# Kernel optimization log

Hardware: AMD Instinct MI355X
Metric: run time of the kernel (lower is better)

The kernel has to match this reference:

```python
import jax, jax.numpy as jnp
import numpy as np

CANDIDATE_SIZE = 1000
IOU_THRESHOLD = 0.5
SCORE_THRESHOLD = 0.3
N_PRIORS = 400000
N_CLASSES = 81


def setup_inputs() -> dict:
    key = jax.random.key(0)
    k1, k2, k3 = jax.random.split(key, 3)
    scores = jax.random.uniform(k1, (1, N_PRIORS, N_CLASSES), dtype=jnp.float32)
    # build valid xyxy boxes in roughly [0, 1.1]
    centers = jax.random.uniform(k2, (1, N_PRIORS, 2), dtype=jnp.float32)
    sizes = jax.random.uniform(k3, (1, N_PRIORS, 2), dtype=jnp.float32) * 0.2 + 0.01
    boxes = jnp.concatenate([centers - sizes / 2, centers + sizes / 2], axis=-1)
    return {"scores": scores, "boxes": boxes}


def _iou_matrix(b):
    # b: [K, 4] xyxy -> [K, K] pairwise IoU
    x1 = jnp.maximum(b[:, None, 0], b[None, :, 0])
    y1 = jnp.maximum(b[:, None, 1], b[None, :, 1])
    x2 = jnp.minimum(b[:, None, 2], b[None, :, 2])
    y2 = jnp.minimum(b[:, None, 3], b[None, :, 3])
    inter = jnp.clip(x2 - x1, 0.0) * jnp.clip(y2 - y1, 0.0)
    area = (b[:, 2] - b[:, 0]) * (b[:, 3] - b[:, 1])
    union = area[:, None] + area[None, :] - inter
    return inter / jnp.maximum(union, 1e-9)


def reference(scores, boxes):
    s = scores[0]  # [N, C]
    b = boxes[0]   # [N, 4]
    cls_scores = s[:, 1:]                    # drop background class
    best = jnp.max(cls_scores, axis=1)       # [N] best foreground score
    labels = jnp.argmax(cls_scores, axis=1)  # [N] 0-based foreground label
    top_scores, top_idx = jax.lax.top_k(best, CANDIDATE_SIZE)  # sorted desc
    top_boxes = b[top_idx]                   # [K, 4]
    top_labels = labels[top_idx]             # [K]
    valid = top_scores > SCORE_THRESHOLD     # score-threshold mask (kept as mask, not filter, for static shapes)

    # batched_nms: offset boxes per class so cross-class IoU is 0
    offset = (top_labels.astype(top_boxes.dtype) * 4.0)[:, None]  # boxes span < 4
    iou = _iou_matrix(top_boxes + offset)    # [K, K]

    idx = jnp.arange(CANDIDATE_SIZE)

    def body(i, keep):
        # greedy suppression: candidates are already score-sorted
        suppress = keep[i] & (iou[i] > IOU_THRESHOLD) & (idx > i)
        return keep & ~suppress

    keep = jax.lax.fori_loop(0, CANDIDATE_SIZE, body, valid)  # [K] bool

    keepf = keep.astype(top_boxes.dtype)
    sel_boxes = top_boxes * keepf[:, None]          # zeroed where suppressed
    sel_probs = top_scores * keepf
    sel_labels = jnp.where(keep, top_labels + 1, 0)  # +1 to restore class ids
    return sel_boxes, sel_labels, sel_probs, keep
```

## Files before the change

### kernel.cpp

```cpp
#include <hip/hip_runtime.h>
#include <stdint.h>

#pragma clang fp contract(off)

#define N_PRIORS   400000
#define NCLS       81
#define TILE       128
#define RED_BLOCKS (N_PRIORS / TILE)
#define HGRID      512
#define CAND_CAP   8192
#define TOPK       1000
#define CM_CAP     448

#define OFF_CTRL    0
#define OFF_HIST0   64
#define OFF_HIST1   1088
#define OFF_HIST2   2112
#define OFF_RNZ     3200
#define OFF_VALID   3328
#define OFF_SLOT    4096
#define OFF_CSCORE  8192
#define OFF_CLABEL  12288
#define OFF_CRAW    16384
#define OFF_OBOX    32768
#define OFF_OAREA   49152
#define OFF_CAND    65536
#define OFF_CM      131072
#define OFF_KEYS    262144
#define OFF_LABELS  (OFF_KEYS + N_PRIORS * 8)

__device__ __forceinline__ uint32_t atomLoadU32(const uint32_t* p) {
  return __hip_atomic_load(p, __ATOMIC_RELAXED, __HIP_MEMORY_SCOPE_AGENT);
}
__device__ __forceinline__ uint64_t atomLoadU64(const uint64_t* p) {
  return __hip_atomic_load(p, __ATOMIC_RELAXED, __HIP_MEMORY_SCOPE_AGENT);
}
__device__ __forceinline__ void atomStoreU64(uint64_t* p, uint64_t v) {
  __hip_atomic_store(p, v, __ATOMIC_RELAXED, __HIP_MEMORY_SCOPE_AGENT);
}
__device__ __forceinline__ void atomStoreU32(uint32_t* p, uint32_t v) {
  __hip_atomic_store(p, v, __ATOMIC_RELAXED, __HIP_MEMORY_SCOPE_AGENT);
}

__device__ __forceinline__ void gload_lds16(const void* g, void* l) {
  __builtin_amdgcn_global_load_lds(
      (const __attribute__((address_space(1))) void*)g,
      (__attribute__((address_space(3))) void*)l, 16, 0, 0);
}

__device__ __forceinline__ void select_digit_wave(const uint32_t* hist, uint32_t k,
                                                  uint32_t prefix, int sh_dig,
                                                  uint32_t* ctrl, int lane) {
  uint32_t h[4];
  #pragma unroll
  for (int t = 0; t < 4; ++t) h[t] = atomLoadU32(&hist[255 - (4 * lane + t)]);
  uint32_t part = h[0] + h[1] + h[2] + h[3];
  uint32_t incl = part;
  #pragma unroll
  for (int d = 1; d < 64; d <<= 1) {
    uint32_t up = __shfl_up(incl, d);
    if (lane >= d) incl += up;
  }
  uint32_t excl = incl - part;
  if (excl < k && k <= incl) {
    uint32_t cum = excl;
    #pragma unroll
    for (int t = 0; t < 4; ++t) {
      if (cum + h[t] >= k) {
        ctrl[0] = prefix | ((uint32_t)(255 - (4 * lane + t)) << sh_dig);
        ctrl[1] = k - cum;
        break;
      }
      cum += h[t];
    }
  }
}

__global__ __launch_bounds__(256) void k_reduce(const float* __restrict__ scores,
                                                uint8_t* __restrict__ ws) {
  __shared__ __align__(16) float s_tile[TILE * NCLS];
  __shared__ uint32_t s_hist[256];
  __shared__ int s_last;
  uint32_t* ctrl  = (uint32_t*)(ws + OFF_CTRL);
  uint32_t* hist0 = (uint32_t*)(ws + OFF_HIST0);
  uint64_t* keys  = (uint64_t*)(ws + OFF_KEYS);
  int32_t*  labs  = (int32_t*)(ws + OFF_LABELS);
  const int tid = threadIdx.x;
  s_hist[tid] = 0;

  const float* src = scores + (size_t)blockIdx.x * (TILE * NCLS);
  {
    const int wave = tid >> 6, lane = tid & 63;
    const char* gbase = (const char*)src + lane * 16;
    char* lbase = (char*)s_tile;
    #pragma unroll
    for (int c = wave; c < 40; c += 4)
      gload_lds16(gbase + c * 1024, lbase + c * 1024);
  }
  if (tid < 32) {
    float4 v = ((const float4*)src)[2560 + tid];
    ((float4*)s_tile)[2560 + tid] = v;
  }
  __syncthreads();

  const int pl = tid >> 1, half = tid & 1;
  const float* row = s_tile + pl * NCLS + 1 + half * 40;
  float best = -1.0f; int lab = 0;
  #pragma unroll
  for (int c = 0; c < 40; ++c) {
    float v = row[c];
    if (v > best) { best = v; lab = c; }
  }
  lab += half * 40;
  float obst = __shfl_xor(best, 1);
  int   olab = __shfl_xor(lab, 1);
  float b0 = half ? obst : best;  int l0 = half ? olab : lab;
  float b1 = half ? best : obst;  int l1 = half ? lab  : olab;
  float fb = (b1 > b0) ? b1 : b0;
  int   fl = (b1 > b0) ? l1 : l0;

  if (half == 0) {
    int p = blockIdx.x * TILE + pl;
    uint32_t bits = __float_as_uint(fb);
    keys[p] = ((uint64_t)bits << 32) | (uint32_t)(~(uint32_t)p);
    labs[p] = fl;
    atomicAdd(&s_hist[bits >> 24], 1u);
  }
  __syncthreads();
  uint32_t h = s_hist[tid];
  if (h) atomicAdd(&hist0[tid], h);
  __syncthreads();
  if (tid == 0) {
    int r = blockIdx.x & 7;
    uint32_t target = (RED_BLOCKS >> 3) + ((uint32_t)r < (RED_BLOCKS & 7) ? 1u : 0u);
    int last = 0;
    if (atomicAdd(&ctrl[8 + r], 1u) == target - 1u)
      last = (atomicAdd(&ctrl[3], 1u) == 7u);
    s_last = last;
  }
  __syncthreads();
  if (s_last && tid < 64)
    select_digit_wave(hist0, TOPK, 0u, 24, ctrl, tid);
}

template <int P>
__global__ __launch_bounds__(256) void k_hist(uint8_t* __restrict__ ws) {
  __shared__ uint32_t s_hist[256];
  __shared__ int s_last;
  uint32_t* ctrl = (uint32_t*)(ws + OFF_CTRL);
  uint32_t* hist = (uint32_t*)(ws + (P == 1 ? OFF_HIST1 : OFF_HIST2));
  const uint64_t* keys = (const uint64_t*)(ws + OFF_KEYS);
  const int tid = threadIdx.x;
  s_hist[tid] = 0;
  __syncthreads();
  const uint32_t prefix = ctrl[0];
  constexpr int SH_MATCH = 32 - 8 * P;
  constexpr int SH_DIG   = 24 - 8 * P;
  const uint32_t pm = prefix >> SH_MATCH;
  for (int i = blockIdx.x * 256 + tid; i < N_PRIORS; i += 256 * HGRID) {
    uint32_t bits = (uint32_t)(keys[i] >> 32);
    if ((bits >> SH_MATCH) == pm) atomicAdd(&s_hist[(bits >> SH_DIG) & 255u], 1u);
  }
  __syncthreads();
  uint32_t h = s_hist[tid];
  if (h) atomicAdd(&hist[tid], h);
  __syncthreads();
  if (tid == 0) s_last = (atomicAdd(&ctrl[3 + P], 1u) == (uint32_t)(HGRID - 1));
  __syncthreads();
  if (s_last && tid < 64)
    select_digit_wave(hist, ctrl[1], prefix, SH_DIG, ctrl, tid);
}

__global__ __launch_bounds__(256) void k_compact(uint8_t* __restrict__ ws) {
  uint32_t* ctrl = (uint32_t*)(ws + OFF_CTRL);
  const uint64_t* keys = (const uint64_t*)(ws + OFF_KEYS);
  uint64_t* cand = (uint64_t*)(ws + OFF_CAND);
  const uint32_t thr = ctrl[0];
  const int tid = threadIdx.x;
  for (int i = blockIdx.x * 256 + tid; i < N_PRIORS; i += 256 * HGRID) {
    uint64_t kk = keys[i];
    if ((uint32_t)(kk >> 32) >= thr) {
      uint32_t pos = atomicAdd(&ctrl[2], 1u);
      if (pos < CAND_CAP) cand[pos] = kk;
    }
  }
}

__global__ __launch_bounds__(256) void k_rank(const float* __restrict__ boxes,
                                              uint8_t* __restrict__ ws) {
  uint32_t* ctrl = (uint32_t*)(ws + OFF_CTRL);
  const uint64_t* cand = (const uint64_t*)(ws + OFF_CAND);
  const int32_t* labs = (const int32_t*)(ws + OFF_LABELS);
  float*   cscore = (float*)(ws + OFF_CSCORE);
  int32_t* clabel = (int32_t*)(ws + OFF_CLABEL);
  float*   craw   = (float*)(ws + OFF_CRAW);
  float*   obox   = (float*)(ws + OFF_OBOX);
  float*   oarea  = (float*)(ws + OFF_OAREA);
  uint64_t* validm = (uint64_t*)(ws + OFF_VALID);
  uint32_t c2 = ctrl[2];
  const uint32_t n = (c2 < CAND_CAP) ? c2 : CAND_CAP;
  const uint32_t j = blockIdx.x;
  if (j >= n) return;
  const uint64_t kj = cand[j];
  const int tid = threadIdx.x;
  uint32_t cnt = 0;
  for (uint32_t i = tid; i < n; i += 256) cnt += (cand[i] > kj) ? 1u : 0u;
  __shared__ uint32_t red[256];
  red[tid] = cnt;
  __syncthreads();
  #pragma unroll
  for (int s = 128; s > 0; s >>= 1) {
    if (tid < s) red[tid] += red[tid + s];
    __syncthreads();
  }
  if (tid == 0) {
    uint32_t rank = red[0];
    if (rank < TOPK) {
      uint32_t idx = ~(uint32_t)kj;
      float sc = __uint_as_float((uint32_t)(kj >> 32));
      int lab = labs[idx];
      float bx0 = boxes[idx * 4 + 0];
      float bx1 = boxes[idx * 4 + 1];
      float bx2 = boxes[idx * 4 + 2];
      float bx3 = boxes[idx * 4 + 3];
      float off = (float)lab * 4.0f;
      float o0 = bx0 + off, o1 = bx1 + off, o2 = bx2 + off, o3 = bx3 + off;
      cscore[rank] = sc;
      clabel[rank] = lab;
      craw[rank * 4 + 0] = bx0; craw[rank * 4 + 1] = bx1;
      craw[rank * 4 + 2] = bx2; craw[rank * 4 + 3] = bx3;
      obox[rank * 4 + 0] = o0;  obox[rank * 4 + 1] = o1;
      obox[rank * 4 + 2] = o2;  obox[rank * 4 + 3] = o3;
      oarea[rank] = (o2 - o0) * (o3 - o1);
      if (sc > 0.3f)
        atomicOr((unsigned long long*)&validm[rank >> 6], 1ull << (rank & 63));
    }
  }
}

__global__ __launch_bounds__(256) void k_iou_nms(float* __restrict__ out,
                                                 uint8_t* __restrict__ ws) {
  __shared__ uint64_t s_words[16];
  __shared__ uint32_t s_slotsh;
  __shared__ int s_last;
  __shared__ uint64_t s_keep[16];
  __shared__ uint16_t s_slot[TOPK];
  __shared__ uint64_t s_cm[CM_CAP * 16];

  uint32_t* ctrl = (uint32_t*)(ws + OFF_CTRL);
  const float* obox  = (const float*)(ws + OFF_OBOX);
  const float* oarea = (const float*)(ws + OFF_OAREA);
  uint64_t* CM  = (uint64_t*)(ws + OFF_CM);
  uint64_t* rnz = (uint64_t*)(ws + OFF_RNZ);
  uint32_t* slotmap = (uint32_t*)(ws + OFF_SLOT);
  const uint64_t* validm = (const uint64_t*)(ws + OFF_VALID);
  const float*   cscore = (const float*)(ws + OFF_CSCORE);
  const int32_t* clabel = (const int32_t*)(ws + OFF_CLABEL);
  const float*   craw   = (const float*)(ws + OFF_CRAW);

  const int i = blockIdx.x;
  const int tid = threadIdx.x;
  const float bi0 = obox[i * 4 + 0], bi1 = obox[i * 4 + 1];
  const float bi2 = obox[i * 4 + 2], bi3 = obox[i * 4 + 3];
  const float ai = oarea[i];
  #pragma unroll
  for (int k = 0; k < 4; ++k) {
    int j = tid + 256 * k;
    const float4 bj = ((const float4*)obox)[j];
    float x1 = fmaxf(bi0, bj.x);
    float y1 = fmaxf(bi1, bj.y);
    float x2 = fminf(bi2, bj.z);
    float y2 = fminf(bi3, bj.w);
    float iw = fmaxf(x2 - x1, 0.0f);
    float ih = fmaxf(y2 - y1, 0.0f);
    float inter = iw * ih;
    float uni = ai + oarea[j] - inter;
    float iou = inter / fmaxf(uni, 1e-9f);
    bool pred = (iou > 0.5f) && (j > i) && (j < TOPK);
    uint64_t m = __ballot(pred);
    if ((tid & 63) == 0) s_words[(tid >> 6) + 4 * k] = m;
  }
  __syncthreads();
  if (tid == 0) {
    uint64_t any = 0;
    #pragma unroll
    for (int w = 0; w < 16; ++w) any |= s_words[w];
    uint32_t sl = 0xFFFFFFFFu;
    if (any) {
      sl = atomicAdd(&ctrl[7], 1u);
      atomicOr((unsigned long long*)&rnz[i >> 6], 1ull << (i & 63));
      atomStoreU32(&slotmap[i], sl + 1u);
    }
    s_slotsh = sl;
  }
  __syncthreads();
  {
    uint32_t sl = s_slotsh;
    if (sl != 0xFFFFFFFFu && tid < 16)
      atomStoreU64(&CM[(size_t)sl * 16 + tid], s_words[tid]);
  }
  __syncthreads();
  if (tid == 0) s_last = (atomicAdd(&ctrl[6], 1u) == (uint32_t)(TOPK - 1));
  __syncthreads();
  if (!s_last) return;

  uint32_t cmcnt = atomLoadU32(&ctrl[7]);
  uint32_t ncm = cmcnt < CM_CAP ? cmcnt : CM_CAP;
  for (int r = tid; r < TOPK; r += 256)
    s_slot[r] = (uint16_t)atomLoadU32(&slotmap[r]);
  for (uint32_t x = tid; x < ncm * 16; x += 256)
    s_cm[x] = atomLoadU64(&CM[x]);
  __syncthreads();

  if (tid < 64) {
    const int lane = tid;
    uint64_t keep = 0, rz = 0;
    if (lane < 16) {
      keep = validm[lane];
      rz = atomLoadU64(&rnz[lane]);
    }
    for (int w = 0; w < 16; ++w) {
      uint64_t rw = __shfl(rz, w);
      int start = 0;
      while (true) {
        uint64_t kw = __shfl(keep, w);
        uint64_t act = kw & rw;
        if (start) act &= (~0ull) << start;
        if (!act) break;
        int il = __builtin_ctzll(act);
        int row = w * 64 + il;
        uint32_t sv = s_slot[row];
        uint64_t m = 0;
        if (lane < 16 && sv) {
          uint32_t s = sv - 1u;
          m = (s < ncm) ? s_cm[s * 16 + lane]
                        : atomLoadU64(&CM[(size_t)s * 16 + lane]);
        }
        keep &= ~m;
        if (il >= 63) break;
        start = il + 1;
      }
    }
    if (lane < 16) s_keep[lane] = keep;
  }
  __syncthreads();

  for (int e = tid; e < 4000; e += 256) {
    int j = e >> 2;
    bool kp = (s_keep[j >> 6] >> (j & 63)) & 1ull;
    out[e] = kp ? craw[e] : 0.0f;
  }
  for (int j = tid; j < TOPK; j += 256) {
    bool kp = (s_keep[j >> 6] >> (j & 63)) & 1ull;
    out[4000 + j] = kp ? (float)(clabel[j] + 1) : 0.0f;
    out[5000 + j] = kp ? cscore[j] : 0.0f;
    out[6000 + j] = kp ? 1.0f : 0.0f;
  }
}

extern "C" void kernel_launch(void* const* d_in, const int* in_sizes, int n_in,
                              void* d_out, int out_size, void* d_ws, size_t ws_size,
                              hipStream_t stream) {
  const float* scores = (const float*)d_in[0];
  const float* boxes  = (const float*)d_in[1];
  float* out = (float*)d_out;
  uint8_t* ws = (uint8_t*)d_ws;

  (void)in_sizes; (void)n_in; (void)out_size; (void)ws_size;

  hipMemsetAsync(d_ws, 0, 65536, stream);
  k_reduce<<<RED_BLOCKS, 256, 0, stream>>>(scores, ws);
  k_hist<1><<<HGRID, 256, 0, stream>>>(ws);
  k_hist<2><<<HGRID, 256, 0, stream>>>(ws);
  k_compact<<<HGRID, 256, 0, stream>>>(ws);
  k_rank<<<CAND_CAP, 256, 0, stream>>>(boxes, ws);
  k_iou_nms<<<TOPK, 256, 0, stream>>>(out, ws);
}
```

Measured before the change: 265.6 us.

## Fuse post-reduce stages into one cooperative kernel with grid barriers

```diff
diff --git a/kernel.cpp b/kernel.cpp
--- a/kernel.cpp
+++ b/kernel.cpp
@@ -11,11 +11,12 @@
 #define CAND_CAP   8192
 #define TOPK       1000
 #define CM_CAP     448
+#define NB         256
 
 #define OFF_CTRL    0
-#define OFF_HIST0   64
-#define OFF_HIST1   1088
-#define OFF_HIST2   2112
+#define OFF_HIST0   128
+#define OFF_HIST1   1152
+#define OFF_HIST2   2176
 #define OFF_RNZ     3200
 #define OFF_VALID   3328
 #define OFF_SLOT    4096
@@ -48,6 +49,23 @@
       (__attribute__((address_space(3))) void*)l, 16, 0, 0);
 }
 
+__device__ __forceinline__ void grid_sync(uint32_t* ctrl, uint32_t phase, int tid) {
+  __syncthreads();
+  if (tid == 0) {
+    uint32_t* cnt = &ctrl[15 + phase];
+    uint32_t* gen = &ctrl[24];
+    uint32_t a = __hip_atomic_fetch_add(cnt, 1u, __ATOMIC_ACQ_REL,
+                                        __HIP_MEMORY_SCOPE_AGENT);
+    if (a == (uint32_t)(NB - 1)) {
+      __hip_atomic_store(gen, phase, __ATOMIC_RELEASE, __HIP_MEMORY_SCOPE_AGENT);
+    } else {
+      while (__hip_atomic_load(gen, __ATOMIC_ACQUIRE, __HIP_MEMORY_SCOPE_AGENT) < phase)
+        __builtin_amdgcn_s_sleep(2);
+    }
+  }
+  __syncthreads();
+}
+
 __device__ __forceinline__ void select_digit_wave(const uint32_t* hist, uint32_t k,
                                                   uint32_t prefix, int sh_dig,
                                                   uint32_t* ctrl, int lane) {
@@ -76,6 +94,38 @@
   }
 }
 
+__device__ __forceinline__ void select_digit_lds(const uint32_t* hist, uint32_t k,
+                                                 uint32_t prefix, int sh_dig,
+                                                 uint32_t* s_sel, int tid) {
+  if (tid < 64) {
+    int lane = tid;
+    uint32_t h[4];
+    #pragma unroll
+    for (int t = 0; t < 4; ++t) h[t] = atomLoadU32(&hist[255 - (4 * lane + t)]);
+    uint32_t part = h[0] + h[1] + h[2] + h[3];
+    uint32_t incl = part;
+    #pragma unroll
+    for (int d = 1; d < 64; d <<= 1) {
+      uint32_t up = __shfl_up(incl, d);
+      if (lane >= d) incl += up;
+    }
+    uint32_t excl = incl - part;
+    if (excl < k && k <= incl) {
+      uint32_t cum = excl;
+      #pragma unroll
+      for (int t = 0; t < 4; ++t) {
+        if (cum + h[t] >= k) {
+          s_sel[0] = prefix | ((uint32_t)(255 - (4 * lane + t)) << sh_dig);
+          s_sel[1] = k - cum;
+          break;
+        }
+        cum += h[t];
+      }
+    }
+  }
+  __syncthreads();
+}
+
 __global__ __launch_bounds__(256) void k_reduce(const float* __restrict__ scores,
                                                 uint8_t* __restrict__ ws) {
   __shared__ __align__(16) float s_tile[TILE * NCLS];
@@ -141,6 +191,215 @@
   __syncthreads();
   if (s_last && tid < 64)
     select_digit_wave(hist0, TOPK, 0u, 24, ctrl, tid);
+}
+
+__global__ __launch_bounds__(256) void k_post(const float* __restrict__ boxes,
+                                              float* __restrict__ out,
+                                              uint8_t* __restrict__ ws) {
+  __shared__ uint32_t s_hist[256];
+  __shared__ uint32_t s_sel[2];
+  __shared__ uint32_t s_red[256];
+  __shared__ uint64_t s_words[16];
+  __shared__ uint32_t s_sl;
+  __shared__ uint64_t s_keep[16];
+  __shared__ uint16_t s_slot[TOPK];
+  __shared__ uint64_t s_cm[CM_CAP * 16];
+
+  uint32_t* ctrl  = (uint32_t*)(ws + OFF_CTRL);
+  uint32_t* hist1 = (uint32_t*)(ws + OFF_HIST1);
+  uint32_t* hist2 = (uint32_t*)(ws + OFF_HIST2);
+  const uint64_t* keys = (const uint64_t*)(ws + OFF_KEYS);
+  const int32_t*  labs = (const int32_t*)(ws + OFF_LABELS);
+  uint64_t* cand = (uint64_t*)(ws + OFF_CAND);
+  float*   cscore = (float*)(ws + OFF_CSCORE);
+  int32_t* clabel = (int32_t*)(ws + OFF_CLABEL);
+  float*   craw   = (float*)(ws + OFF_CRAW);
+  float*   obox   = (float*)(ws + OFF_OBOX);
+  float*   oarea  = (float*)(ws + OFF_OAREA);
+  uint64_t* validm = (uint64_t*)(ws + OFF_VALID);
+  uint64_t* CM  = (uint64_t*)(ws + OFF_CM);
+  uint64_t* rnz = (uint64_t*)(ws + OFF_RNZ);
+  uint32_t* slotmap = (uint32_t*)(ws + OFF_SLOT);
+
+  const int tid = threadIdx.x;
+  const int bid = blockIdx.x;
+
+  s_hist[tid] = 0;
+  __syncthreads();
+  const uint32_t prefix0 = ctrl[0];
+  const uint32_t krem0   = ctrl[1];
+  const uint32_t pm1 = prefix0 >> 24;
+  for (int i = bid * 256 + tid; i < N_PRIORS; i += NB * 256) {
+    uint32_t bits = (uint32_t)(keys[i] >> 32);
+    if ((bits >> 24) == pm1) atomicAdd(&s_hist[(bits >> 16) & 255u], 1u);
+  }
+  __syncthreads();
+  if (s_hist[tid]) atomicAdd(&hist1[tid], s_hist[tid]);
+  grid_sync(ctrl, 1, tid);
+  select_digit_lds(hist1, krem0, prefix0, 16, s_sel, tid);
+  const uint32_t prefix1 = s_sel[0], krem1 = s_sel[1];
+  __syncthreads();
+
+  s_hist[tid] = 0;
+  __syncthreads();
+  const uint32_t pm2 = prefix1 >> 16;
+  for (int i = bid * 256 + tid; i < N_PRIORS; i += NB * 256) {
+    uint32_t bits = (uint32_t)(keys[i] >> 32);
+    if ((bits >> 16) == pm2) atomicAdd(&s_hist[(bits >> 8) & 255u], 1u);
+  }
+  __syncthreads();
+  if (s_hist[tid]) atomicAdd(&hist2[tid], s_hist[tid]);
+  grid_sync(ctrl, 2, tid);
+  select_digit_lds(hist2, krem1, prefix1, 8, s_sel, tid);
+  const uint32_t thr = s_sel[0];
+
+  for (int i = bid * 256 + tid; i < N_PRIORS; i += NB * 256) {
+    uint64_t kk = keys[i];
+    if ((uint32_t)(kk >> 32) >= thr) {
+      uint32_t pos = atomicAdd(&ctrl[2], 1u);
+      if (pos < CAND_CAP) cand[pos] = kk;
+    }
+  }
+  grid_sync(ctrl, 3, tid);
+
+  {
+    uint32_t c2 = ctrl[2];
+    const uint32_t n = (c2 < CAND_CAP) ? c2 : CAND_CAP;
+    for (uint32_t j = bid; j < n; j += NB) {
+      const uint64_t kj = cand[j];
+      uint32_t cnt = 0;
+      for (uint32_t i = tid; i < n; i += 256) cnt += (cand[i] > kj) ? 1u : 0u;
+      s_red[tid] = cnt;
+      __syncthreads();
+      #pragma unroll
+      for (int s = 128; s > 0; s >>= 1) {
+        if (tid < s) s_red[tid] += s_red[tid + s];
+        __syncthreads();
+      }
+      if (tid == 0) {
+        uint32_t rank = s_red[0];
+        if (rank < TOPK) {
+          uint32_t idx = ~(uint32_t)kj;
+          float sc = __uint_as_float((uint32_t)(kj >> 32));
+          int lab = labs[idx];
+          float bx0 = boxes[idx * 4 + 0];
+          float bx1 = boxes[idx * 4 + 1];
+          float bx2 = boxes[idx * 4 + 2];
+          float bx3 = boxes[idx * 4 + 3];
+          float off = (float)lab * 4.0f;
+          float o0 = bx0 + off, o1 = bx1 + off, o2 = bx2 + off, o3 = bx3 + off;
+          cscore[rank] = sc;
+          clabel[rank] = lab;
+          craw[rank * 4 + 0] = bx0; craw[rank * 4 + 1] = bx1;
+          craw[rank * 4 + 2] = bx2; craw[rank * 4 + 3] = bx3;
+          obox[rank * 4 + 0] = o0;  obox[rank * 4 + 1] = o1;
+          obox[rank * 4 + 2] = o2;  obox[rank * 4 + 3] = o3;
+          oarea[rank] = (o2 - o0) * (o3 - o1);
+          if (sc > 0.3f)
+            atomicOr((unsigned long long*)&validm[rank >> 6], 1ull << (rank & 63));
+        }
+      }
+      __syncthreads();
+    }
+  }
+  grid_sync(ctrl, 4, tid);
+
+  for (int r = 0; r < 4; ++r) {
+    const int i = bid * 4 + r;
+    if (i < TOPK) {
+      const float bi0 = obox[i * 4 + 0], bi1 = obox[i * 4 + 1];
+      const float bi2 = obox[i * 4 + 2], bi3 = obox[i * 4 + 3];
+      const float ai = oarea[i];
+      #pragma unroll
+      for (int k = 0; k < 4; ++k) {
+        int j = tid + 256 * k;
+        const float4 bj = ((const float4*)obox)[j];
+        float x1 = fmaxf(bi0, bj.x);
+        float y1 = fmaxf(bi1, bj.y);
+        float x2 = fminf(bi2, bj.z);
+        float y2 = fminf(bi3, bj.w);
+        float iw = fmaxf(x2 - x1, 0.0f);
+        float ih = fmaxf(y2 - y1, 0.0f);
+        float inter = iw * ih;
+        float uni = ai + oarea[j] - inter;
+        float iou = inter / fmaxf(uni, 1e-9f);
+        bool pred = (iou > 0.5f) && (j > i) && (j < TOPK);
+        uint64_t m = __ballot(pred);
+        if ((tid & 63) == 0) s_words[(tid >> 6) + 4 * k] = m;
+      }
+    }
+    __syncthreads();
+    if (i < TOPK && tid == 0) {
+      uint64_t any = 0;
+      #pragma unroll
+      for (int w = 0; w < 16; ++w) any |= s_words[w];
+      uint32_t sl = 0xFFFFFFFFu;
+      if (any) {
+        sl = atomicAdd(&ctrl[7], 1u);
+        atomicOr((unsigned long long*)&rnz[i >> 6], 1ull << (i & 63));
+        slotmap[i] = sl + 1u;
+      }
+      s_sl = sl;
+    }
+    __syncthreads();
+    if (i < TOPK && s_sl != 0xFFFFFFFFu && tid < 16)
+      CM[(size_t)s_sl * 16 + tid] = s_words[tid];
+    __syncthreads();
+  }
+  grid_sync(ctrl, 5, tid);
+
+  if (bid != 0) return;
+  uint32_t cmcnt = ctrl[7];
+  uint32_t ncm = cmcnt < CM_CAP ? cmcnt : CM_CAP;
+  for (int r2 = tid; r2 < TOPK; r2 += 256)
+    s_slot[r2] = (uint16_t)slotmap[r2];
+  for (uint32_t x = tid; x < ncm * 16; x += 256)
+    s_cm[x] = CM[x];
+  __syncthreads();
+
+  if (tid < 64) {
+    const int lane = tid;
+    uint64_t keep = 0, rz = 0;
+    if (lane < 16) {
+      keep = validm[lane];
+      rz = rnz[lane];
+    }
+    for (int w = 0; w < 16; ++w) {
+      uint64_t rw = __shfl(rz, w);
+      int start = 0;
+      while (true) {
+        uint64_t kw = __shfl(keep, w);
+        uint64_t act = kw & rw;
+        if (start) act &= (~0ull) << start;
+        if (!act) break;
+        int il = __builtin_ctzll(act);
+        int row = w * 64 + il;
+        uint32_t sv = s_slot[row];
+        uint64_t m = 0;
+        if (lane < 16 && sv) {
+          uint32_t s = sv - 1u;
+          m = (s < ncm) ? s_cm[s * 16 + lane] : CM[(size_t)s * 16 + lane];
+        }
+        keep &= ~m;
+        if (il >= 63) break;
+        start = il + 1;
+      }
+    }
+    if (lane < 16) s_keep[lane] = keep;
+  }
+  __syncthreads();
+
+  for (int e = tid; e < 4000; e += 256) {
+    int j = e >> 2;
+    bool kp = (s_keep[j >> 6] >> (j & 63)) & 1ull;
+    out[e] = kp ? craw[e] : 0.0f;
+  }
+  for (int j = tid; j < TOPK; j += 256) {
+    bool kp = (s_keep[j >> 6] >> (j & 63)) & 1ull;
+    out[4000 + j] = kp ? (float)(clabel[j] + 1) : 0.0f;
+    out[5000 + j] = kp ? cscore[j] : 0.0f;
+    out[6000 + j] = kp ? 1.0f : 0.0f;
+  }
 }
 
 template <int P>
@@ -370,9 +629,16 @@
 
   hipMemsetAsync(d_ws, 0, 65536, stream);
   k_reduce<<<RED_BLOCKS, 256, 0, stream>>>(scores, ws);
-  k_hist<1><<<HGRID, 256, 0, stream>>>(ws);
-  k_hist<2><<<HGRID, 256, 0, stream>>>(ws);
-  k_compact<<<HGRID, 256, 0, stream>>>(ws);
-  k_rank<<<CAND_CAP, 256, 0, stream>>>(boxes, ws);
-  k_iou_nms<<<TOPK, 256, 0, stream>>>(out, ws);
-}
+
+  void* args[] = {(void*)&boxes, (void*)&out, (void*)&ws};
+  hipError_t err = hipLaunchCooperativeKernel(reinterpret_cast<void*>(k_post),
+                                              dim3(NB), dim3(256), args, 0, stream);
+  if (err != hipSuccess) {
+    (void)hipGetLastError();
+    k_hist<1><<<HGRID, 256, 0, stream>>>(ws);
+    k_hist<2><<<HGRID, 256, 0, stream>>>(ws);
+    k_compact<<<HGRID, 256, 0, stream>>>(ws);
+    k_rank<<<CAND_CAP, 256, 0, stream>>>(boxes, ws);
+    k_iou_nms<<<TOPK, 256, 0, stream>>>(out, ws);
+  }
+}
```

Measured after the change: 372.7 us. 40.3% more time.

## Replace three-pass radix select with single 16-bit histogram on complemented scores

Applied to the files above, without the earlier changes.

```diff
diff --git a/kernel.cpp b/kernel.cpp
--- a/kernel.cpp
+++ b/kernel.cpp
@@ -13,9 +13,6 @@
 #define CM_CAP     448
 
 #define OFF_CTRL    0
-#define OFF_HIST0   64
-#define OFF_HIST1   1088
-#define OFF_HIST2   2112
 #define OFF_RNZ     3200
 #define OFF_VALID   3328
 #define OFF_SLOT    4096
@@ -24,9 +21,10 @@
 #define OFF_CRAW    16384
 #define OFF_OBOX    32768
 #define OFF_OAREA   49152
-#define OFF_CAND    65536
-#define OFF_CM      131072
-#define OFF_KEYS    262144
+#define OFF_HIST16  65536
+#define OFF_CAND    327680
+#define OFF_CM      393216
+#define OFF_KEYS    524288
 #define OFF_LABELS  (OFF_KEYS + N_PRIORS * 8)
 
 __device__ __forceinline__ uint32_t atomLoadU32(const uint32_t* p) {
@@ -48,45 +46,23 @@
       (__attribute__((address_space(3))) void*)l, 16, 0, 0);
 }
 
-__device__ __forceinline__ void select_digit_wave(const uint32_t* hist, uint32_t k,
-                                                  uint32_t prefix, int sh_dig,
-                                                  uint32_t* ctrl, int lane) {
-  uint32_t h[4];
-  #pragma unroll
-  for (int t = 0; t < 4; ++t) h[t] = atomLoadU32(&hist[255 - (4 * lane + t)]);
-  uint32_t part = h[0] + h[1] + h[2] + h[3];
-  uint32_t incl = part;
-  #pragma unroll
-  for (int d = 1; d < 64; d <<= 1) {
-    uint32_t up = __shfl_up(incl, d);
-    if (lane >= d) incl += up;
-  }
-  uint32_t excl = incl - part;
-  if (excl < k && k <= incl) {
-    uint32_t cum = excl;
-    #pragma unroll
-    for (int t = 0; t < 4; ++t) {
-      if (cum + h[t] >= k) {
-        ctrl[0] = prefix | ((uint32_t)(255 - (4 * lane + t)) << sh_dig);
-        ctrl[1] = k - cum;
-        break;
-      }
-      cum += h[t];
-    }
-  }
+__device__ __forceinline__ uint32_t cbits(float s) {
+  float c = 1.0f - s;
+  return __float_as_uint(c);
 }
 
 __global__ __launch_bounds__(256) void k_reduce(const float* __restrict__ scores,
                                                 uint8_t* __restrict__ ws) {
   __shared__ __align__(16) float s_tile[TILE * NCLS];
   __shared__ uint32_t s_hist[256];
+  __shared__ uint32_t s_wt[4];
+  __shared__ uint32_t s_win, s_excl;
   __shared__ int s_last;
-  uint32_t* ctrl  = (uint32_t*)(ws + OFF_CTRL);
-  uint32_t* hist0 = (uint32_t*)(ws + OFF_HIST0);
-  uint64_t* keys  = (uint64_t*)(ws + OFF_KEYS);
-  int32_t*  labs  = (int32_t*)(ws + OFF_LABELS);
+  uint32_t* ctrl   = (uint32_t*)(ws + OFF_CTRL);
+  uint32_t* hist16 = (uint32_t*)(ws + OFF_HIST16);
+  uint64_t* keys   = (uint64_t*)(ws + OFF_KEYS);
+  int32_t*  labs   = (int32_t*)(ws + OFF_LABELS);
   const int tid = threadIdx.x;
-  s_hist[tid] = 0;
 
   const float* src = scores + (size_t)blockIdx.x * (TILE * NCLS);
   {
@@ -124,11 +100,8 @@
     uint32_t bits = __float_as_uint(fb);
     keys[p] = ((uint64_t)bits << 32) | (uint32_t)(~(uint32_t)p);
     labs[p] = fl;
-    atomicAdd(&s_hist[bits >> 24], 1u);
-  }
-  __syncthreads();
-  uint32_t h = s_hist[tid];
-  if (h) atomicAdd(&hist0[tid], h);
+    atomicAdd(&hist16[cbits(fb) >> 16], 1u);
+  }
   __syncthreads();
   if (tid == 0) {
     int r = blockIdx.x & 7;
@@ -139,47 +112,70 @@
     s_last = last;
   }
   __syncthreads();
-  if (s_last && tid < 64)
-    select_digit_wave(hist0, TOPK, 0u, 24, ctrl, tid);
-}
-
-template <int P>
-__global__ __launch_bounds__(256) void k_hist(uint8_t* __restrict__ ws) {
-  __shared__ uint32_t s_hist[256];
-  __shared__ int s_last;
-  uint32_t* ctrl = (uint32_t*)(ws + OFF_CTRL);
-  uint32_t* hist = (uint32_t*)(ws + (P == 1 ? OFF_HIST1 : OFF_HIST2));
-  const uint64_t* keys = (const uint64_t*)(ws + OFF_KEYS);
-  const int tid = threadIdx.x;
-  s_hist[tid] = 0;
-  __syncthreads();
-  const uint32_t prefix = ctrl[0];
-  constexpr int SH_MATCH = 32 - 8 * P;
-  constexpr int SH_DIG   = 24 - 8 * P;
-  const uint32_t pm = prefix >> SH_MATCH;
-  for (int i = blockIdx.x * 256 + tid; i < N_PRIORS; i += 256 * HGRID) {
-    uint32_t bits = (uint32_t)(keys[i] >> 32);
-    if ((bits >> SH_MATCH) == pm) atomicAdd(&s_hist[(bits >> SH_DIG) & 255u], 1u);
-  }
-  __syncthreads();
-  uint32_t h = s_hist[tid];
-  if (h) atomicAdd(&hist[tid], h);
-  __syncthreads();
-  if (tid == 0) s_last = (atomicAdd(&ctrl[3 + P], 1u) == (uint32_t)(HGRID - 1));
-  __syncthreads();
-  if (s_last && tid < 64)
-    select_digit_wave(hist, ctrl[1], prefix, SH_DIG, ctrl, tid);
+  if (!s_last) return;
+
+  {
+    const int lane = tid & 63, wid = tid >> 6;
+    const int cbase = 256 * tid;
+    uint32_t csum = 0;
+    for (int b = 0; b < 256; ++b) csum += atomLoadU32(&hist16[cbase + b]);
+    uint32_t incl = csum;
+    #pragma unroll
+    for (int d = 1; d < 64; d <<= 1) {
+      uint32_t up = __shfl_up(incl, d);
+      if (lane >= d) incl += up;
+    }
+    if (lane == 63) s_wt[wid] = incl;
+    __syncthreads();
+    uint32_t woff = 0;
+    #pragma unroll
+    for (int w = 0; w < 4; ++w) if (w < wid) woff += s_wt[w];
+    incl += woff;
+    uint32_t excl = incl - csum;
+    if (excl < TOPK && TOPK <= incl) { s_win = tid; s_excl = excl; }
+    __syncthreads();
+    const int winbase = 256 * s_win;
+    s_hist[tid] = atomLoadU32(&hist16[winbase + tid]);
+    __syncthreads();
+    if (tid < 64) {
+      const uint32_t k2 = TOPK - s_excl;
+      uint32_t h[4];
+      #pragma unroll
+      for (int t = 0; t < 4; ++t) h[t] = s_hist[4 * tid + t];
+      uint32_t part = h[0] + h[1] + h[2] + h[3];
+      uint32_t incl2 = part;
+      #pragma unroll
+      for (int d = 1; d < 64; d <<= 1) {
+        uint32_t up = __shfl_up(incl2, d);
+        if (tid >= d) incl2 += up;
+      }
+      uint32_t excl2 = incl2 - part;
+      if (excl2 < k2 && k2 <= incl2) {
+        uint32_t cum = excl2;
+        #pragma unroll
+        for (int t = 0; t < 4; ++t) {
+          if (cum + h[t] >= k2) {
+            uint32_t B = (uint32_t)winbase + 4 * tid + t;
+            atomStoreU32(&ctrl[0], (B + 1u) << 16);
+            break;
+          }
+          cum += h[t];
+        }
+      }
+    }
+  }
 }
 
 __global__ __launch_bounds__(256) void k_compact(uint8_t* __restrict__ ws) {
   uint32_t* ctrl = (uint32_t*)(ws + OFF_CTRL);
   const uint64_t* keys = (const uint64_t*)(ws + OFF_KEYS);
   uint64_t* cand = (uint64_t*)(ws + OFF_CAND);
-  const uint32_t thr = ctrl[0];
+  const uint32_t thrc = ctrl[0];
   const int tid = threadIdx.x;
   for (int i = blockIdx.x * 256 + tid; i < N_PRIORS; i += 256 * HGRID) {
     uint64_t kk = keys[i];
-    if ((uint32_t)(kk >> 32) >= thr) {
+    float s = __uint_as_float((uint32_t)(kk >> 32));
+    if (cbits(s) < thrc) {
       uint32_t pos = atomicAdd(&ctrl[2], 1u);
       if (pos < CAND_CAP) cand[pos] = kk;
     }
@@ -368,10 +364,8 @@
 
   (void)in_sizes; (void)n_in; (void)out_size; (void)ws_size;
 
-  hipMemsetAsync(d_ws, 0, 65536, stream);
+  hipMemsetAsync(d_ws, 0, OFF_CAND, stream);
   k_reduce<<<RED_BLOCKS, 256, 0, stream>>>(scores, ws);
-  k_hist<1><<<HGRID, 256, 0, stream>>>(ws);
-  k_hist<2><<<HGRID, 256, 0, stream>>>(ws);
   k_compact<<<HGRID, 256, 0, stream>>>(ws);
   k_rank<<<CAND_CAP, 256, 0, stream>>>(boxes, ws);
   k_iou_nms<<<TOPK, 256, 0, stream>>>(out, ws);
```

New measurement: 402.4 us. +51.5%, slower.
